# Kernel optimization log

Measured on AMD Instinct MI355X. Metric: run time of the kernel, lower is better.

The kernel has to match this reference:

```python
import jax, jax.numpy as jnp
import numpy as np

DIM = 256
NUM_HEADS = 8
HEAD_DIM = 64
NUM_MEM_KV = 4
HIDDEN = NUM_HEADS * HEAD_DIM  # 512


def rmsnorm(x, g):
    # F.normalize(x, dim=1) * g * sqrt(C)
    c = x.shape[1]
    n = jnp.sqrt(jnp.sum(x * x, axis=1, keepdims=True))
    xn = x / jnp.maximum(n, 1e-12)
    return xn * g * (c ** 0.5)


def setup_inputs() -> dict:
    key = jax.random.key(0)
    ks = jax.random.split(key, 7)
    b, h, w = 16, 64, 64
    x = jax.random.normal(ks[0], (b, DIM, h, w), dtype=jnp.float32)
    g_in = jnp.ones((1, DIM, 1, 1), dtype=jnp.float32)
    w_qkv = jax.random.normal(ks[1], (HIDDEN * 3, DIM), dtype=jnp.float32) * (1.0 / np.sqrt(DIM))
    mem_kv = jax.random.normal(ks[2], (2, NUM_HEADS, HEAD_DIM, NUM_MEM_KV), dtype=jnp.float32)
    w_out = jax.random.normal(ks[3], (DIM, HIDDEN), dtype=jnp.float32) * (1.0 / np.sqrt(HIDDEN))
    b_out = jax.random.normal(ks[4], (DIM,), dtype=jnp.float32) * 0.01
    g_out = jnp.ones((1, DIM, 1, 1), dtype=jnp.float32)
    return {"x": x, "g_in": g_in, "w_qkv": w_qkv, "mem_kv": mem_kv,
            "w_out": w_out, "b_out": b_out, "g_out": g_out}


def reference(x, g_in, w_qkv, mem_kv, w_out, b_out, g_out):
    b, c, h, w = x.shape
    scale = HEAD_DIM ** (-0.5)
    xn = rmsnorm(x, g_in)
    # 1x1 conv (no bias) as GEMM: [b, 3*hidden, h, w]
    qkv = jnp.einsum('bcxy,oc->boxy', xn, w_qkv)
    q, k, v = jnp.split(qkv, 3, axis=1)
    # b (heads d) x y -> b heads d n
    def to_heads(t):
        return t.reshape(b, NUM_HEADS, HEAD_DIM, h * w)
    q, k, v = to_heads(q), to_heads(k), to_heads(v)
    mem_k = jnp.broadcast_to(mem_kv[0], (b, NUM_HEADS, HEAD_DIM, NUM_MEM_KV))
    mem_v = jnp.broadcast_to(mem_kv[1], (b, NUM_HEADS, HEAD_DIM, NUM_MEM_KV))
    k = jnp.concatenate([mem_k, k], axis=-1)
    v = jnp.concatenate([mem_v, v], axis=-1)
    q = jax.nn.softmax(q, axis=-2) * scale   # softmax over head_dim
    k = jax.nn.softmax(k, axis=-1)           # softmax over sequence
    context = jnp.einsum('bhdn,bhen->bhde', k, v)  # [b,h,d,d] per-head context
    out = jnp.einsum('bhde,bhdn->bhen', context, q)  # [b,h,d,n]
    out = out.reshape(b, HIDDEN, h, w)
    out = jnp.einsum('bcxy,oc->boxy', out, w_out) + b_out[None, :, None, None]
    return rmsnorm(out, g_out)
```

## Files before the change

kernel.cpp:

```cpp
#include <hip/hip_runtime.h>
#include <hip/hip_bf16.h>

typedef __hip_bfloat16 bf16;
typedef short bf16x8 __attribute__((ext_vector_type(8)));
typedef float f32x4 __attribute__((ext_vector_type(4)));

#define PTOT  65536
#define NPOS  4096
#define CIN   256
#define HID   512
#define HD    64

__device__ __forceinline__ float us2f(unsigned short u) {
    return __uint_as_float(((unsigned int)u) << 16);
}
__device__ __forceinline__ float ldf(const void* p, size_t i, bool bf) {
    return bf ? us2f(((const unsigned short*)p)[i]) : ((const float*)p)[i];
}
__device__ __forceinline__ unsigned short f2bs(float v) {
    __hip_bfloat16 h = __float2bfloat16(v);
    return *reinterpret_cast<unsigned short*>(&h);
}
__device__ __forceinline__ void gld16(const void* g, void* s) {
    __builtin_amdgcn_global_load_lds(
        (const __attribute__((address_space(1))) unsigned int*)g,
        (__attribute__((address_space(3))) unsigned int*)s, 16, 0, 0);
}

__global__ __launch_bounds__(256) void k_detect(const unsigned* __restrict__ x,
                                                int* __restrict__ flag) {
    int t = threadIdx.x;
    unsigned w = x[(size_t)t * 997];
    unsigned e7 = (w >> 8) & 0x7f;
    __shared__ int s[256];
    s[t] = (e7 >= 58 && e7 <= 66) ? 1 : 0;
    __syncthreads();
    for (int k = 128; k > 0; k >>= 1) { if (t < k) s[t] += s[t + k]; __syncthreads(); }
    if (t == 0) flag[0] = (s[0] >= 128) ? 1 : 0;
}

__global__ void k_relay(const int* __restrict__ src, int* __restrict__ dst) {
    dst[0] = src[0];
}

__global__ __launch_bounds__(256) void k_cvt(const void* __restrict__ src,
        unsigned short* __restrict__ dst, int n, const int* __restrict__ flag) {
    bool bf = flag[0] != 0;
    int i = blockIdx.x * 256 + threadIdx.x;
    if (i < n) dst[i] = f2bs(ldf(src, i, bf));
}

template<bool BF>
__device__ __forceinline__ void norm_xn_body(const void* __restrict__ x,
        const void* __restrict__ g, unsigned short* __restrict__ xn,
        float* __restrict__ smem)
{
    float* xs   = smem;
    float* gS   = smem + 17216;
    float* red2 = smem + 17472;
    float* sS   = smem + 18496;
    const int t = threadIdx.x;
    const int p0 = blockIdx.x * 64;
    const int b = p0 >> 12;
    const int posbase = p0 & 4095;
    gS[t] = ldf(g, t, BF);
    __syncthreads();
    const int pl4 = (t & 15) * 4;
    const int crow = t >> 4;
    const size_t xbase = ((size_t)b * CIN) << 12;
    float ssq[4] = {0.f, 0.f, 0.f, 0.f};
    #pragma unroll
    for (int rr = 0; rr < 16; ++rr) {
        int c = rr * 16 + crow;
        float v[4];
        if (BF) {
            ushort4 u = *(const ushort4*)((const unsigned short*)x + xbase +
                                          ((size_t)c << 12) + posbase + pl4);
            v[0] = us2f(u.x); v[1] = us2f(u.y); v[2] = us2f(u.z); v[3] = us2f(u.w);
        } else {
            float4 f = *(const float4*)((const float*)x + xbase +
                                        ((size_t)c << 12) + posbase + pl4);
            v[0] = f.x; v[1] = f.y; v[2] = f.z; v[3] = f.w;
        }
        float gv = gS[c];
        float* row = xs + (c >> 6) * 4304 + (c & 63) * 67;
        #pragma unroll
        for (int e = 0; e < 4; ++e) {
            ssq[e] += v[e] * v[e];
            row[pl4 + e] = v[e] * gv;
        }
    }
    #pragma unroll
    for (int e = 0; e < 4; ++e) red2[crow * 64 + pl4 + e] = ssq[e];
    __syncthreads();
    if (t < 64) {
        float tot = 0.f;
        #pragma unroll
        for (int j = 0; j < 16; ++j) tot += red2[j * 64 + t];
        sS[t] = 16.0f / fmaxf(sqrtf(tot), 1e-12f);
    }
    __syncthreads();
    const int pr = t >> 2, c0 = (t & 3) * 64;
    const float sc = sS[pr];
    const float* base = xs + (t & 3) * 4304 + pr;
    unsigned short* dst = &xn[(size_t)(p0 + pr) * 256 + c0];
    #pragma unroll
    for (int q = 0; q < 4; ++q) {
        unsigned short tmp[16];
        #pragma unroll
        for (int j = 0; j < 16; ++j)
            tmp[j] = f2bs(base[(q * 16 + j) * 67] * sc);
        *(uint4*)(dst + q * 16)     = ((uint4*)tmp)[0];
        *(uint4*)(dst + q * 16 + 8) = ((uint4*)tmp)[1];
    }
}
__global__ __launch_bounds__(256) void k_norm_xn(
        const void* __restrict__ x, const void* __restrict__ g,
        unsigned short* __restrict__ xn, const int* __restrict__ flag)
{
    __shared__ float smem[18560];
    if (flag[0]) norm_xn_body<true>(x, g, xn, smem);
    else         norm_xn_body<false>(x, g, xn, smem);
}

template<int KTOT, bool BIAS, int OSTRIDE>
__global__ __launch_bounds__(256) void k_mfma(
        const bf16* __restrict__ Am, const bf16* __restrict__ Bm,
        const void* __restrict__ bias, bf16* __restrict__ C,
        const int* __restrict__ flag)
{
    __shared__ __align__(16) unsigned short As[128 * 32];
    __shared__ __align__(16) unsigned short Bs[128 * 32];
    const int tid = threadIdx.x;
    const int wv = tid >> 6, lane = tid & 63;
    const int quad = lane >> 4, l16 = lane & 15;
    const int wm = wv >> 1, wn = wv & 1;
    const int m0 = blockIdx.y * 128, n0 = blockIdx.x * 128;
    f32x4 acc[4][4] = {};
    const bf16* gA = Am + (size_t)(m0 + (tid >> 2)) * KTOT + (tid & 3) * 8;
    const bf16* gB = Bm + (size_t)(n0 + (tid >> 2)) * KTOT + (tid & 3) * 8;
    unsigned short* lA = As + wv * 512;
    unsigned short* lB = Bs + wv * 512;
    for (int k0 = 0; k0 < KTOT; k0 += 32) {
        gld16(gA + k0, lA);
        gld16(gA + (size_t)64 * KTOT + k0, lA + 2048);
        gld16(gB + k0, lB);
        gld16(gB + (size_t)64 * KTOT + k0, lB + 2048);
        __syncthreads();
        bf16x8 bfr[4];
        #pragma unroll
        for (int j = 0; j < 4; ++j)
            bfr[j] = *(const bf16x8*)&Bs[(wn * 64 + j * 16 + l16) * 32 + quad * 8];
        #pragma unroll
        for (int i = 0; i < 4; ++i) {
            bf16x8 af = *(const bf16x8*)&As[(wm * 64 + i * 16 + l16) * 32 + quad * 8];
            #pragma unroll
            for (int j = 0; j < 4; ++j)
                acc[i][j] = __builtin_amdgcn_mfma_f32_16x16x32_bf16(af, bfr[j], acc[i][j], 0, 0, 0);
        }
        __syncthreads();
    }
    bool bf = BIAS ? (flag[0] != 0) : false;
    #pragma unroll
    for (int i = 0; i < 4; ++i) {
        int row = m0 + wm * 64 + i * 16 + quad * 4;
        #pragma unroll
        for (int r = 0; r < 4; ++r) {
            float bv = BIAS ? ldf(bias, row + r, bf) : 0.0f;
            #pragma unroll
            for (int j = 0; j < 4; ++j) {
                int col = n0 + wn * 64 + j * 16 + l16;
                C[(size_t)(row + r) * OSTRIDE + col] = __float2bfloat16(acc[i][j][r] + bv);
            }
        }
    }
}

__global__ __launch_bounds__(512, 4) void k_kvgemm(
        const bf16* __restrict__ Am, const bf16* __restrict__ Bm,
        bf16* __restrict__ C)
{
    __shared__ __align__(16) char smem[65536];
    const int t = threadIdx.x;
    const int w = t >> 6, lane = t & 63;
    const int quad = lane >> 4, l16 = lane & 15;
    const int wm = w >> 1, wn = w & 1;
    const int bid = blockIdx.x;
    const int c  = (bid & 7) | ((bid >> 6) << 3);
    const int mt = (bid >> 3) & 7;
    const int m0 = mt * 128;
    const size_t cbase = (size_t)c * 1024;

    const int srow = t >> 5;
    const int sks  = (t & 31) ^ (srow & 7);

    #pragma unroll
    for (int q = 0; q < 8; ++q)
        gld16(Am + (size_t)(m0 + q * 16 + srow) * 256 + sks * 8,
              smem + q * 8192 + w * 1024);
    asm volatile("s_waitcnt vmcnt(0)" ::: "memory");
    __builtin_amdgcn_s_barrier();
    asm volatile("" ::: "memory");

    bf16x8 af[2][8];
    #pragma unroll
    for (int i = 0; i < 2; ++i) {
        int row = wm * 32 + i * 16 + l16;
        #pragma unroll
        for (int kk = 0; kk < 8; ++kk)
            af[i][kk] = *(const bf16x8*)(smem + row * 512 +
                         (((kk * 4 + quad) ^ (row & 7)) << 4));
    }
    asm volatile("s_waitcnt lgkmcnt(0)" ::: "memory");
    __builtin_amdgcn_s_barrier();
    asm volatile("" ::: "memory");

    #pragma unroll
    for (int q = 0; q < 4; ++q)
        gld16(Bm + (cbase + q * 16 + srow) * 256 + sks * 8,
              smem + q * 8192 + w * 1024);
    #pragma unroll
    for (int q = 0; q < 4; ++q)
        gld16(Bm + (cbase + 64 + q * 16 + srow) * 256 + sks * 8,
              smem + 32768 + q * 8192 + w * 1024);

    for (int s = 0; s < 16; ++s) {
        if (s > 0) {
            asm volatile("" ::: "memory");
            __builtin_amdgcn_s_barrier();
            asm volatile("" ::: "memory");
            if (s + 1 < 16) {
                #pragma unroll
                for (int q = 0; q < 4; ++q)
                    gld16(Bm + (cbase + (size_t)(s + 1) * 64 + q * 16 + srow) * 256 + sks * 8,
                          smem + ((s + 1) & 1) * 32768 + q * 8192 + w * 1024);
            }
        }
        if (s == 0)      asm volatile("s_waitcnt vmcnt(4)"  ::: "memory");
        else if (s < 15) asm volatile("s_waitcnt vmcnt(20)" ::: "memory");
        else             asm volatile("s_waitcnt vmcnt(16)" ::: "memory");
        __builtin_amdgcn_s_barrier();
        asm volatile("" ::: "memory");

        const char* Bbuf = smem + (s & 1) * 32768;
        f32x4 acc[2][2] = {};
        #pragma unroll
        for (int kk = 0; kk < 8; ++kk) {
            bf16x8 bfr[2];
            #pragma unroll
            for (int j = 0; j < 2; ++j) {
                int row = wn * 32 + j * 16 + l16;
                bfr[j] = *(const bf16x8*)(Bbuf + row * 512 +
                          (((kk * 4 + quad) ^ (row & 7)) << 4));
            }
            #pragma unroll
            for (int i = 0; i < 2; ++i)
                #pragma unroll
                for (int j = 0; j < 2; ++j)
                    acc[i][j] = __builtin_amdgcn_mfma_f32_16x16x32_bf16(af[i][kk], bfr[j], acc[i][j], 0, 0, 0);
        }
        #pragma unroll
        for (int i = 0; i < 2; ++i) {
            #pragma unroll
            for (int r = 0; r < 4; ++r) {
                int row = m0 + wm * 32 + i * 16 + quad * 4 + r;
                size_t col = cbase + (size_t)s * 64 + wn * 32;
                #pragma unroll
                for (int j = 0; j < 2; ++j)
                    C[(size_t)row * PTOT + col + j * 16 + l16] = __float2bfloat16(acc[i][j][r]);
            }
        }
    }
}

__global__ __launch_bounds__(512, 2) void k_qapply(
        const bf16* __restrict__ xn, const bf16* __restrict__ wq,
        const unsigned short* __restrict__ ct_bf,
        unsigned short* __restrict__ oat_pe)
{
    __shared__ __align__(16) char smem[163840];
    const int t = threadIdx.x;
    const int w = t >> 6, lane = t & 63;
    const int quad = lane >> 4, l16 = lane & 15;
    const int wm = w >> 1, wn = w & 1;
    const int bid = blockIdx.x;
    const int hp = (bid >> 3) & 3;
    const int c  = (bid & 7) | ((bid >> 5) << 3);
    const int n0 = hp * 128;
    const size_t P0 = (size_t)c * 1024;
    const int b = c >> 2;
    const int srow = t >> 5, sks = (t & 31) ^ (srow & 7);

    #pragma unroll
    for (int k = 0; k < 2; ++k) {
        int u = k * 512 + t;
        int hh = u >> 9, rem = u & 511, e = rem >> 3, sl = rem & 7;
        gld16(ct_bf + (size_t)(b * 8 + hp * 2 + hh) * 4096 + e * 64 + ((sl ^ (e & 7)) * 8),
              smem + 81920 + k * 8192 + w * 1024);
    }
    #pragma unroll
    for (int q = 0; q < 8; ++q)
        gld16(wq + (size_t)(n0 + q * 16 + srow) * 256 + sks * 8,
              smem + q * 8192 + w * 1024);
    #pragma unroll
    for (int q = 0; q < 4; ++q)
        gld16(xn + (P0 + q * 16 + srow) * 256 + sks * 8,
              smem + 98304 + q * 8192 + w * 1024);
    #pragma unroll
    for (int q = 0; q < 4; ++q)
        gld16(xn + (P0 + 64 + q * 16 + srow) * 256 + sks * 8,
              smem + 131072 + q * 8192 + w * 1024);

    asm volatile("s_waitcnt vmcnt(8)" ::: "memory");
    __builtin_amdgcn_s_barrier();
    asm volatile("" ::: "memory");

    bf16x8 wqf[4][8];
    #pragma unroll
    for (int j = 0; j < 4; ++j) {
        int row = wn * 64 + j * 16 + l16;
        #pragma unroll
        for (int kk = 0; kk < 8; ++kk)
            wqf[j][kk] = *(const bf16x8*)(smem + row * 512 +
                          (((kk * 4 + quad) ^ (row & 7)) << 4));
    }

    unsigned short* qsm = (unsigned short*)(smem + 65536);

    for (int s = 0; s < 16; ++s) {
        if (s > 0) {
            asm volatile("" ::: "memory");
            __builtin_amdgcn_s_barrier();
            asm volatile("" ::: "memory");
            if (s + 1 < 16) {
                #pragma unroll
                for (int q = 0; q < 4; ++q)
                    gld16(xn + (P0 + (size_t)(s + 1) * 64 + q * 16 + srow) * 256 + sks * 8,
                          smem + 98304 + ((s + 1) & 1) * 32768 + q * 8192 + w * 1024);
            }
        }
        if (s == 0)      asm volatile("s_waitcnt vmcnt(4)"  ::: "memory");
        else if (s < 15) asm volatile("s_waitcnt vmcnt(20)" ::: "memory");
        else             asm volatile("s_waitcnt vmcnt(16)" ::: "memory");
        __builtin_amdgcn_s_barrier();
        asm volatile("" ::: "memory");

        const char* Bbuf = smem + 98304 + (s & 1) * 32768;
        f32x4 acc[4] = {};
        #pragma unroll
        for (int kk = 0; kk < 8; ++kk) {
            int row = wm * 16 + l16;
            bf16x8 xf = *(const bf16x8*)(Bbuf + row * 512 +
                          (((kk * 4 + quad) ^ (row & 7)) << 4));
            #pragma unroll
            for (int j = 0; j < 4; ++j)
                acc[j] = __builtin_amdgcn_mfma_f32_16x16x32_bf16(xf, wqf[j][kk], acc[j], 0, 0, 0);
        }

        #pragma unroll
        for (int r = 0; r < 4; ++r) {
            float m = fmaxf(fmaxf(acc[0][r], acc[1][r]), fmaxf(acc[2][r], acc[3][r]));
            m = fmaxf(m, __shfl_xor(m, 1));
            m = fmaxf(m, __shfl_xor(m, 2));
            m = fmaxf(m, __shfl_xor(m, 4));
            m = fmaxf(m, __shfl_xor(m, 8));
            float ev[4], sum = 0.f;
            #pragma unroll
            for (int j = 0; j < 4; ++j) { ev[j] = __expf(acc[j][r] - m); sum += ev[j]; }
            sum += __shfl_xor(sum, 1);
            sum += __shfl_xor(sum, 2);
            sum += __shfl_xor(sum, 4);
            sum += __shfl_xor(sum, 8);
            float inv = 0.125f / sum;
            int pos = wm * 16 + quad * 4 + r;
            #pragma unroll
            for (int j = 0; j < 4; ++j) {
                int ch = wn * 64 + j * 16 + l16;
                qsm[pos * 128 + (((ch >> 3) ^ (pos & 7)) << 3) + (ch & 7)] = f2bs(ev[j] * inv);
            }
        }

        f32x4 acc2[4] = {};
        #pragma unroll
        for (int kk = 0; kk < 2; ++kk) {
            int row = wm * 16 + l16;
            bf16x8 qf = *(const bf16x8*)(smem + 65536 + row * 256 +
                         (((wn * 8 + kk * 4 + quad) ^ (row & 7)) << 4));
            #pragma unroll
            for (int j = 0; j < 4; ++j) {
                int e = j * 16 + l16;
                bf16x8 cf = *(const bf16x8*)(smem + 81920 + wn * 8192 + e * 128 +
                             (((kk * 4 + quad) ^ (e & 7)) << 4));
                acc2[j] = __builtin_amdgcn_mfma_f32_16x16x32_bf16(qf, cf, acc2[j], 0, 0, 0);
            }
        }
        #pragma unroll
        for (int j = 0; j < 4; ++j)
            #pragma unroll
            for (int r = 0; r < 4; ++r) {
                size_t prow = P0 + (size_t)s * 64 + wm * 16 + quad * 4 + r;
                oat_pe[prow * HID + n0 + wn * 64 + j * 16 + l16] = f2bs(acc2[j][r]);
            }
    }
}

__global__ __launch_bounds__(256) void k_kstats(
        const bf16* __restrict__ kv, const void* __restrict__ memkv,
        float* __restrict__ rowmax, float* __restrict__ rowinv,
        const int* __restrict__ flag)
{
    bool bf = flag[0] != 0;
    int r = blockIdx.x;
    int b = r >> 9, hd = r & 511;
    const unsigned short* krow = (const unsigned short*)kv + (size_t)hd * PTOT + b * NPOS;
    int t = threadIdx.x;
    float vals[16];
    float m = -1e30f;
    #pragma unroll
    for (int i = 0; i < 16; ++i) {
        vals[i] = us2f(krow[t + (i << 8)]);
        m = fmaxf(m, vals[i]);
    }
    float mv = (t < 4) ? ldf(memkv, hd * 4 + t, bf) : -1e30f;
    m = fmaxf(m, mv);
    __shared__ float red[256];
    red[t] = m; __syncthreads();
    for (int s = 128; s > 0; s >>= 1) {
        if (t < s) red[t] = fmaxf(red[t], red[t + s]);
        __syncthreads();
    }
    float M = red[0]; __syncthreads();
    float sum = 0.f;
    #pragma unroll
    for (int i = 0; i < 16; ++i) sum += __expf(vals[i] - M);
    if (t < 4) sum += __expf(mv - M);
    red[t] = sum; __syncthreads();
    for (int s = 128; s > 0; s >>= 1) {
        if (t < s) red[t] += red[t + s];
        __syncthreads();
    }
    if (t == 0) { rowmax[r] = M; rowinv[r] = 1.0f / red[0]; }
}

__global__ __launch_bounds__(256) void k_context_mfma(
        const bf16* __restrict__ kv, const void* __restrict__ memkv,
        const float* __restrict__ rowmax, const float* __restrict__ rowinv,
        float* __restrict__ ctpart, const int* __restrict__ flag)
{
    bool bf = flag[0] != 0;
    int bh = blockIdx.x, chunk = blockIdx.y;
    int b = bh >> 3, h = bh & 7;
    __shared__ __align__(16) unsigned short As[4][64 * 32];
    __shared__ __align__(16) unsigned short Bs[4][64 * 32];
    __shared__ float rmS[64], riS[64];
    const int tid = threadIdx.x;
    if (tid < 64) {
        rmS[tid] = rowmax[(b << 9) + (h << 6) + tid];
        riS[tid] = rowinv[(b << 9) + (h << 6) + tid];
    }
    __syncthreads();
    const int wv = tid >> 6, lane = tid & 63;
    const int quad = lane >> 4, l16 = lane & 15;
    const int wm = wv >> 1, wn = wv & 1;
    const int krow = tid >> 2, kseg = tid & 3;
    const float rm = rmS[krow], ri = riS[krow];
    const unsigned short* kbase = (const unsigned short*)kv + (size_t)(h * HD) * PTOT + b * NPOS + chunk * 1024;
    const unsigned short* vbase = (const unsigned short*)kv + (size_t)(HID + h * HD) * PTOT + b * NPOS + chunk * 1024;
    f32x4 acc[2][2] = {};
    for (int s = 0; s < 8; ++s) {
        int nb = s * 128;
        #pragma unroll
        for (int kk = 0; kk < 4; ++kk) {
            uint4 u = *(const uint4*)(kbase + (size_t)krow * PTOT + nb + kk * 32 + kseg * 8);
            unsigned short out[8];
            const unsigned short* us = (const unsigned short*)&u;
            #pragma unroll
            for (int e = 0; e < 8; ++e)
                out[e] = f2bs(__expf(us2f(us[e]) - rm) * ri);
            *(uint4*)&As[kk][krow * 32 + kseg * 8] = *(uint4*)out;
        }
        #pragma unroll
        for (int kk = 0; kk < 4; ++kk)
            gld16(vbase + (size_t)(wv * 16 + (lane >> 2)) * PTOT + nb + kk * 32 + (lane & 3) * 8,
                  &Bs[kk][wv * 512]);
        __syncthreads();
        #pragma unroll
        for (int kk = 0; kk < 4; ++kk) {
            bf16x8 bfr[2];
            #pragma unroll
            for (int j = 0; j < 2; ++j)
                bfr[j] = *(const bf16x8*)&Bs[kk][(wn * 32 + j * 16 + l16) * 32 + quad * 8];
            #pragma unroll
            for (int i = 0; i < 2; ++i) {
                bf16x8 af = *(const bf16x8*)&As[kk][(wm * 32 + i * 16 + l16) * 32 + quad * 8];
                #pragma unroll
                for (int j = 0; j < 2; ++j)
                    acc[i][j] = __builtin_amdgcn_mfma_f32_16x16x32_bf16(af, bfr[j], acc[i][j], 0, 0, 0);
            }
        }
        __syncthreads();
    }
    if (chunk == 0) {
        float mv[2][4];
        #pragma unroll
        for (int j = 0; j < 2; ++j) {
            int e = wn * 32 + j * 16 + l16;
            #pragma unroll
            for (int mm = 0; mm < 4; ++mm)
                mv[j][mm] = ldf(memkv, 2048 + ((h << 6) + e) * 4 + mm, bf);
        }
        #pragma unroll
        for (int i = 0; i < 2; ++i) {
            #pragma unroll
            for (int r = 0; r < 4; ++r) {
                int d = wm * 32 + i * 16 + quad * 4 + r;
                #pragma unroll
                for (int mm = 0; mm < 4; ++mm) {
                    float kw = __expf(ldf(memkv, ((h << 6) + d) * 4 + mm, bf) - rmS[d]) * riS[d];
                    #pragma unroll
                    for (int j = 0; j < 2; ++j)
                        acc[i][j][r] = fmaf(kw, mv[j][mm], acc[i][j][r]);
                }
            }
        }
    }
    float* outp = ctpart + (size_t)(chunk * 128 + bh) * 4096;
    #pragma unroll
    for (int i = 0; i < 2; ++i) {
        #pragma unroll
        for (int r = 0; r < 4; ++r) {
            int d = wm * 32 + i * 16 + quad * 4 + r;
            #pragma unroll
            for (int j = 0; j < 2; ++j) {
                int e = wn * 32 + j * 16 + l16;
                outp[d * 64 + e] = acc[i][j][r];
            }
        }
    }
}

__global__ __launch_bounds__(256) void k_ctsum(
        const float* __restrict__ ctpart, unsigned short* __restrict__ ct_bf)
{
    int bh = blockIdx.x, t = threadIdx.x;
    int i0 = t * 16;
    int e = i0 >> 6, d0 = i0 & 63;
    unsigned short tmp[16];
    #pragma unroll
    for (int j = 0; j < 16; ++j) {
        int d = d0 + j;
        float s = 0.f;
        #pragma unroll
        for (int c = 0; c < 4; ++c)
            s += ctpart[(size_t)(c * 128 + bh) * 4096 + d * 64 + e];
        tmp[j] = f2bs(s);
    }
    unsigned short* dst = ct_bf + (size_t)bh * 4096 + i0;
    *(uint4*)dst = ((uint4*)tmp)[0];
    *(uint4*)(dst + 8) = ((uint4*)tmp)[1];
}

template<bool BF>
__device__ __forceinline__ void rmsout_body(const unsigned short* __restrict__ pre,
        const void* __restrict__ g, void* __restrict__ out, float* __restrict__ smem)
{
    float* gS   = smem;
    float* red2 = smem + 256;
    float* sS   = smem + 1280;
    const int t = threadIdx.x;
    const int p0 = blockIdx.x * 64;
    const int b = p0 >> 12;
    const int posbase = p0 & 4095;
    gS[t] = ldf(g, t, BF);
    const int pl4 = (t & 15) * 4;
    const int crow = t >> 4;
    const unsigned short* pbase = pre + p0 + pl4;
    ushort4 u[16];
    float ssq[4] = {0.f, 0.f, 0.f, 0.f};
    #pragma unroll
    for (int rr = 0; rr < 16; ++rr) {
        int c = rr * 16 + crow;
        u[rr] = *(const ushort4*)(pbase + (size_t)c * PTOT);
        float v0 = us2f(u[rr].x), v1 = us2f(u[rr].y), v2 = us2f(u[rr].z), v3 = us2f(u[rr].w);
        ssq[0] += v0 * v0; ssq[1] += v1 * v1; ssq[2] += v2 * v2; ssq[3] += v3 * v3;
    }
    #pragma unroll
    for (int e = 0; e < 4; ++e) red2[crow * 64 + pl4 + e] = ssq[e];
    __syncthreads();
    if (t < 64) {
        float tot = 0.f;
        #pragma unroll
        for (int j = 0; j < 16; ++j) tot += red2[j * 64 + t];
        sS[t] = 16.0f / fmaxf(sqrtf(tot), 1e-12f);
    }
    __syncthreads();
    const float s0 = sS[pl4], s1 = sS[pl4 + 1], s2 = sS[pl4 + 2], s3 = sS[pl4 + 3];
    #pragma unroll
    for (int rr = 0; rr < 16; ++rr) {
        int c = rr * 16 + crow;
        float gv = gS[c];
        float v0 = us2f(u[rr].x) * s0 * gv;
        float v1 = us2f(u[rr].y) * s1 * gv;
        float v2 = us2f(u[rr].z) * s2 * gv;
        float v3 = us2f(u[rr].w) * s3 * gv;
        size_t oi = ((size_t)(b * CIN + c) << 12) + posbase + pl4;
        if (BF) {
            ushort4 o;
            o.x = f2bs(v0); o.y = f2bs(v1); o.z = f2bs(v2); o.w = f2bs(v3);
            *(ushort4*)((unsigned short*)out + oi) = o;
        } else {
            float4 o; o.x = v0; o.y = v1; o.z = v2; o.w = v3;
            *(float4*)((float*)out + oi) = o;
        }
    }
}
__global__ __launch_bounds__(256) void k_rmsnorm_out(
        const unsigned short* __restrict__ pre, const void* __restrict__ g,
        void* __restrict__ out, const int* __restrict__ flag)
{
    __shared__ float smem[1344];
    if (flag[0]) rmsout_body<true>(pre, g, out, smem);
    else         rmsout_body<false>(pre, g, out, smem);
}

extern "C" void kernel_launch(void* const* d_in, const int* in_sizes, int n_in,
                              void* d_out, int out_size, void* d_ws, size_t ws_size,
                              hipStream_t stream) {
    const void* x     = d_in[0];
    const void* g_in  = d_in[1];
    const void* w_qkv = d_in[2];
    const void* memkv = d_in[3];
    const void* w_out = d_in[4];
    const void* b_out = d_in[5];
    const void* g_out = d_in[6];

    char* ws = (char*)d_ws;
    bf16*           kv     = (bf16*)ws;
    unsigned short* oat_pe = (unsigned short*)(ws + 67108864);
    unsigned short* pre    = (unsigned short*)ws;
    int*            flagB  = (int*)(ws + 50331648);

    char* ob = (char*)d_out;
    float*          ctpart = (float*)ob;
    float*          rowmax = (float*)(ob + 8388608);
    float*          rowinv = (float*)(ob + 8421376);
    int*            flagA  = (int*)(ob + 8454144);
    unsigned short* wq_b   = (unsigned short*)(ob + 9437184);
    unsigned short* wout_b = (unsigned short*)(ob + 10485760);
    unsigned short* ct_bf  = (unsigned short*)(ob + 11010048);
    unsigned short* xn     = (unsigned short*)(ob + 12582912);

    k_detect<<<1, 256, 0, stream>>>((const unsigned*)x, flagA);

    k_cvt<<<1536, 256, 0, stream>>>(w_qkv, wq_b, 1536 * 256, flagA);
    k_cvt<<<512, 256, 0, stream>>>(w_out, wout_b, 256 * 512, flagA);

    k_norm_xn<<<1024, 256, 0, stream>>>(x, g_in, xn, flagA);

    k_kvgemm<<<512, 512, 0, stream>>>(
        (const bf16*)(wq_b + (size_t)512 * CIN), (const bf16*)xn, kv);

    k_kstats<<<8192, 256, 0, stream>>>(kv, memkv, rowmax, rowinv, flagA);

    dim3 gctx(128, 4);
    k_context_mfma<<<gctx, 256, 0, stream>>>(kv, memkv, rowmax, rowinv, ctpart, flagA);

    k_ctsum<<<128, 256, 0, stream>>>(ctpart, ct_bf);

    k_qapply<<<256, 512, 0, stream>>>(
        (const bf16*)xn, (const bf16*)wq_b, ct_bf, oat_pe);

    dim3 go(512, 2);
    k_mfma<HID, true, PTOT><<<go, 256, 0, stream>>>(
        (const bf16*)wout_b, (const bf16*)oat_pe, b_out, (bf16*)pre, flagA);

    k_relay<<<1, 1, 0, stream>>>(flagA, flagB);

    k_rmsnorm_out<<<1024, 256, 0, stream>>>(pre, g_out, d_out, flagB);
}
```

Measured before the change: 318.7 us.

## Split q-apply kernel to one head per block with smaller LDS footprint

The q-apply kernel now processes a single head (64 channels) per block with 256 threads instead of two heads with 512 threads, launching 512 blocks instead of 256. LDS use is cut from 160KB to 80KB by reusing the weight staging region for the double-buffered x tiles after weights move to registers. This aims to raise occupancy and the block count on the device, at the cost of loading each x tile twice as often across blocks (once per head instead of once per head pair).

```diff
diff --git a/kernel.cpp b/kernel.cpp
--- a/kernel.cpp
+++ b/kernel.cpp
@@ -273,59 +273,64 @@
     }
 }
 
-__global__ __launch_bounds__(512, 2) void k_qapply(
+#define QSM_OFF 65536
+#define CT_OFF  73728
+__global__ __launch_bounds__(256, 2) void k_qapply(
         const bf16* __restrict__ xn, const bf16* __restrict__ wq,
         const unsigned short* __restrict__ ct_bf,
         unsigned short* __restrict__ oat_pe)
 {
-    __shared__ __align__(16) char smem[163840];
+    __shared__ __align__(16) char smem[81920];
     const int t = threadIdx.x;
     const int w = t >> 6, lane = t & 63;
     const int quad = lane >> 4, l16 = lane & 15;
-    const int wm = w >> 1, wn = w & 1;
     const int bid = blockIdx.x;
-    const int hp = (bid >> 3) & 3;
-    const int c  = (bid & 7) | ((bid >> 5) << 3);
-    const int n0 = hp * 128;
+    const int h = (bid >> 3) & 7;
+    const int c = (bid & 7) | ((bid >> 6) << 3);
+    const int n0 = h * HD;
     const size_t P0 = (size_t)c * 1024;
-    const int b = c >> 2;
-    const int srow = t >> 5, sks = (t & 31) ^ (srow & 7);
-
+    const int b = (int)(P0 >> 12);
+    const int srow = t >> 5;
+    const int sks  = (t & 31) ^ srow;
+
+    #pragma unroll
+    for (int q = 0; q < 8; ++q)
+        gld16(wq + (size_t)(n0 + q * 8 + srow) * 256 + sks * 8,
+              smem + q * 4096 + w * 1024);
     #pragma unroll
     for (int k = 0; k < 2; ++k) {
-        int u = k * 512 + t;
-        int hh = u >> 9, rem = u & 511, e = rem >> 3, sl = rem & 7;
-        gld16(ct_bf + (size_t)(b * 8 + hp * 2 + hh) * 4096 + e * 64 + ((sl ^ (e & 7)) * 8),
-              smem + 81920 + k * 8192 + w * 1024);
-    }
-    #pragma unroll
-    for (int q = 0; q < 8; ++q)
-        gld16(wq + (size_t)(n0 + q * 16 + srow) * 256 + sks * 8,
-              smem + q * 8192 + w * 1024);
-    #pragma unroll
-    for (int q = 0; q < 4; ++q)
-        gld16(xn + (P0 + q * 16 + srow) * 256 + sks * 8,
-              smem + 98304 + q * 8192 + w * 1024);
-    #pragma unroll
-    for (int q = 0; q < 4; ++q)
-        gld16(xn + (P0 + 64 + q * 16 + srow) * 256 + sks * 8,
-              smem + 131072 + q * 8192 + w * 1024);
-
-    asm volatile("s_waitcnt vmcnt(8)" ::: "memory");
+        int u = k * 256 + t;
+        int e = u >> 3, sl = u & 7;
+        gld16(ct_bf + (size_t)(b * 8 + h) * 4096 + e * 64 + ((sl ^ (e & 7)) * 8),
+              smem + CT_OFF + k * 4096 + w * 1024);
+    }
+    asm volatile("s_waitcnt vmcnt(2)" ::: "memory");
     __builtin_amdgcn_s_barrier();
     asm volatile("" ::: "memory");
 
     bf16x8 wqf[4][8];
     #pragma unroll
     for (int j = 0; j < 4; ++j) {
-        int row = wn * 64 + j * 16 + l16;
+        int row = j * 16 + l16;
         #pragma unroll
         for (int kk = 0; kk < 8; ++kk)
             wqf[j][kk] = *(const bf16x8*)(smem + row * 512 +
                           (((kk * 4 + quad) ^ (row & 7)) << 4));
     }
-
-    unsigned short* qsm = (unsigned short*)(smem + 65536);
+    asm volatile("s_waitcnt lgkmcnt(0)" ::: "memory");
+    __builtin_amdgcn_s_barrier();
+    asm volatile("" ::: "memory");
+
+    #pragma unroll
+    for (int q = 0; q < 8; ++q)
+        gld16(xn + (P0 + q * 8 + srow) * 256 + sks * 8,
+              smem + q * 4096 + w * 1024);
+    #pragma unroll
+    for (int q = 0; q < 8; ++q)
+        gld16(xn + (P0 + 64 + q * 8 + srow) * 256 + sks * 8,
+              smem + 32768 + q * 4096 + w * 1024);
+
+    unsigned short* qsm = (unsigned short*)(smem + QSM_OFF);
 
     for (int s = 0; s < 16; ++s) {
         if (s > 0) {
@@ -334,22 +339,22 @@
             asm volatile("" ::: "memory");
             if (s + 1 < 16) {
                 #pragma unroll
-                for (int q = 0; q < 4; ++q)
-                    gld16(xn + (P0 + (size_t)(s + 1) * 64 + q * 16 + srow) * 256 + sks * 8,
-                          smem + 98304 + ((s + 1) & 1) * 32768 + q * 8192 + w * 1024);
-            }
-        }
-        if (s == 0)      asm volatile("s_waitcnt vmcnt(4)"  ::: "memory");
-        else if (s < 15) asm volatile("s_waitcnt vmcnt(20)" ::: "memory");
+                for (int q = 0; q < 8; ++q)
+                    gld16(xn + (P0 + (size_t)(s + 1) * 64 + q * 8 + srow) * 256 + sks * 8,
+                          smem + ((s + 1) & 1) * 32768 + q * 4096 + w * 1024);
+            }
+        }
+        if (s == 0)      asm volatile("s_waitcnt vmcnt(8)"  ::: "memory");
+        else if (s < 15) asm volatile("s_waitcnt vmcnt(24)" ::: "memory");
         else             asm volatile("s_waitcnt vmcnt(16)" ::: "memory");
         __builtin_amdgcn_s_barrier();
         asm volatile("" ::: "memory");
 
-        const char* Bbuf = smem + 98304 + (s & 1) * 32768;
+        const char* Bbuf = smem + (s & 1) * 32768;
         f32x4 acc[4] = {};
         #pragma unroll
         for (int kk = 0; kk < 8; ++kk) {
-            int row = wm * 16 + l16;
+            int row = w * 16 + l16;
             bf16x8 xf = *(const bf16x8*)(Bbuf + row * 512 +
                           (((kk * 4 + quad) ^ (row & 7)) << 4));
             #pragma unroll
@@ -372,24 +377,24 @@
             sum += __shfl_xor(sum, 4);
             sum += __shfl_xor(sum, 8);
             float inv = 0.125f / sum;
-            int pos = wm * 16 + quad * 4 + r;
+            int pos = w * 16 + quad * 4 + r;
             #pragma unroll
             for (int j = 0; j < 4; ++j) {
-                int ch = wn * 64 + j * 16 + l16;
-                qsm[pos * 128 + (((ch >> 3) ^ (pos & 7)) << 3) + (ch & 7)] = f2bs(ev[j] * inv);
+                int ch = j * 16 + l16;
+                qsm[pos * 64 + (((ch >> 3) ^ (pos & 7)) << 3) + (ch & 7)] = f2bs(ev[j] * inv);
             }
         }
 
         f32x4 acc2[4] = {};
         #pragma unroll
         for (int kk = 0; kk < 2; ++kk) {
-            int row = wm * 16 + l16;
-            bf16x8 qf = *(const bf16x8*)(smem + 65536 + row * 256 +
-                         (((wn * 8 + kk * 4 + quad) ^ (row & 7)) << 4));
+            int row = w * 16 + l16;
+            bf16x8 qf = *(const bf16x8*)(smem + QSM_OFF + row * 128 +
+                         (((kk * 4 + quad) ^ (row & 7)) << 4));
             #pragma unroll
             for (int j = 0; j < 4; ++j) {
                 int e = j * 16 + l16;
-                bf16x8 cf = *(const bf16x8*)(smem + 81920 + wn * 8192 + e * 128 +
+                bf16x8 cf = *(const bf16x8*)(smem + CT_OFF + e * 128 +
                              (((kk * 4 + quad) ^ (e & 7)) << 4));
                 acc2[j] = __builtin_amdgcn_mfma_f32_16x16x32_bf16(qf, cf, acc2[j], 0, 0, 0);
             }
@@ -398,8 +403,8 @@
         for (int j = 0; j < 4; ++j)
             #pragma unroll
             for (int r = 0; r < 4; ++r) {
-                size_t prow = P0 + (size_t)s * 64 + wm * 16 + quad * 4 + r;
-                oat_pe[prow * HID + n0 + wn * 64 + j * 16 + l16] = f2bs(acc2[j][r]);
+                size_t prow = P0 + (size_t)s * 64 + w * 16 + quad * 4 + r;
+                oat_pe[prow * HID + n0 + j * 16 + l16] = f2bs(acc2[j][r]);
             }
     }
 }
@@ -667,7 +672,7 @@
 
     k_ctsum<<<128, 256, 0, stream>>>(ctpart, ct_bf);
 
-    k_qapply<<<256, 512, 0, stream>>>(
+    k_qapply<<<512, 256, 0, stream>>>(
         (const bf16*)xn, (const bf16*)wq_b, ct_bf, oat_pe);
 
     dim3 go(512, 2);
```

Measured after the change: 321.8 us. About the same (+1.0%).
